# Kernel tuning notes

Hardware: AMD Instinct MI355X
Metric: run time of the kernel (lower is better)

## Reference

```python
import jax, jax.numpy as jnp
import numpy as np

B, H, W, DIM = 2, 128, 128, 256
HEADS, DHEAD = 16, 64
INNER = HEADS * DHEAD  # 1024
EPS = 1e-5  # BatchNorm eps


def _dwconv(x, w, groups):
    # x: [b, c_in, h, w], w: [c_out, c_in//groups, 3, 3], pad=1, stride=1
    return jax.lax.conv_general_dilated(
        x, w, window_strides=(1, 1), padding=((1, 1), (1, 1)),
        dimension_numbers=('NCHW', 'OIHW', 'NCHW'), feature_group_count=groups)


def _bn(x, gamma, beta, mean, var):
    # inference-mode BatchNorm2d over channel dim of NCHW
    inv = gamma * jax.lax.rsqrt(var + EPS)
    return (x - mean[None, :, None, None]) * inv[None, :, None, None] + beta[None, :, None, None]


def setup_inputs() -> dict:
    key = jax.random.key(0)
    ks = jax.random.split(key, 12)
    d = {}
    d['x_in'] = jax.random.normal(ks[0], (B, H, W, DIM), jnp.float32)
    def convw(k, cout):
        return jax.random.normal(k, (cout, 1, 3, 3), jnp.float32) * 0.1
    d['wq'] = convw(ks[1], INNER)
    d['wk'] = convw(ks[2], INNER)
    d['wv'] = convw(ks[3], INNER)
    for name, k in zip(('q', 'k', 'v'), (ks[4], ks[5], ks[6])):
        k0, k1 = jax.random.split(k)
        d[f'bn{name}_g'] = 1.0 + 0.1 * jax.random.normal(k0, (INNER,), jnp.float32)
        d[f'bn{name}_b'] = 0.05 * jax.random.normal(k1, (INNER,), jnp.float32)
        d[f'bn{name}_m'] = jnp.zeros((INNER,), jnp.float32)
        d[f'bn{name}_v'] = jnp.ones((INNER,), jnp.float32)
    d['rescale'] = jnp.ones((HEADS, 1, 1), jnp.float32)
    d['proj_w'] = jax.random.normal(ks[7], (DIM, INNER), jnp.float32) / np.sqrt(INNER).astype(np.float32)
    d['proj_b'] = jnp.zeros((DIM,), jnp.float32)
    d['pos_w1'] = convw(ks[8], DIM)
    d['pos_w2'] = convw(ks[9], DIM)
    return d


def _forward(x_in, wq, wk, wv,
             bnq_g, bnq_b, bnq_m, bnq_v,
             bnk_g, bnk_b, bnk_m, bnk_v,
             bnv_g, bnv_b, bnv_m, bnv_v,
             rescale, proj_w, proj_b, pos_w1, pos_w2):
    b, h, w, c = x_in.shape
    n = h * w
    x = jnp.transpose(x_in, (0, 3, 1, 2))  # [b, c, h, w]

    def proj_path(wc, g, be, m, va):
        y = _bn(_dwconv(x, wc, c), g, be, m, va)        # [b, INNER, h, w]
        return y.reshape(b, INNER, n).transpose(0, 2, 1)  # 'b c h w -> b (h w) c'

    q_inp = proj_path(wq, bnq_g, bnq_b, bnq_m, bnq_v)  # [b, n, INNER]
    k_inp = proj_path(wk, bnk_g, bnk_b, bnk_m, bnk_v)
    v_inp = proj_path(wv, bnv_g, bnv_b, bnv_m, bnv_v)

    def to_heads(t):
        # 'b n (h d) -> b h n d' then transpose(-2,-1) -> [b, heads, d, n]
        return t.reshape(b, n, HEADS, DHEAD).transpose(0, 2, 3, 1)

    q = to_heads(q_inp)
    k = to_heads(k_inp)
    v = to_heads(v_inp)
    # L2 normalize along token dim (last axis), torch F.normalize eps=1e-12
    q = q / jnp.clip(jnp.linalg.norm(q, axis=-1, keepdims=True), 1e-12)
    k = k / jnp.clip(jnp.linalg.norm(k, axis=-1, keepdims=True), 1e-12)

    attn = jnp.einsum('bhdn,bhen->bhde', k, q) * rescale[None]  # [b, heads, d, d]
    attn = jax.nn.softmax(attn, axis=-1)
    xo = jnp.einsum('bhde,bhen->bhdn', attn, v)  # [b, heads, d, n]
    # faithful to torch: raw reshape of [b, heads, d, n] -> [b, n, heads*d]
    xo = xo.reshape(b, n, HEADS * DHEAD)

    out_c = (xo @ proj_w.T + proj_b).reshape(b, h, w, c)

    vp = (v_inp @ proj_w.T + proj_b).reshape(b, h, w, c).transpose(0, 3, 1, 2)
    pe = _dwconv(jax.nn.gelu(_dwconv(vp, pos_w1, c), approximate=False), pos_w2, c)
    out_p = pe.transpose(0, 2, 3, 1)
    return out_c + out_p


def reference(x_in, wq, wk, wv,
              bnq_g, bnq_b, bnq_m, bnq_v,
              bnk_g, bnk_b, bnk_m, bnk_v,
              bnv_g, bnv_b, bnv_m, bnv_v,
              rescale, proj_w, proj_b, pos_w1, pos_w2):
    return _forward(x_in, wq, wk, wv,
                    bnq_g, bnq_b, bnq_m, bnq_v,
                    bnk_g, bnk_b, bnk_m, bnk_v,
                    bnv_g, bnv_b, bnv_m, bnv_v,
                    rescale, proj_w, proj_b, pos_w1, pos_w2)
```

## Files before the change

### kernel.cpp

```cpp
#include <hip/hip_runtime.h>

#define NTOK 16384
#define CDIM 256
#define INNER 1024
#define WW 128
#define HH 128

typedef unsigned short bf16_t;
typedef __bf16 bf16x8 __attribute__((ext_vector_type(8)));
typedef float f32x4 __attribute__((ext_vector_type(4)));

__device__ __forceinline__ float bf2f(bf16_t u) {
    union { unsigned int i; float f; } x;
    x.i = ((unsigned int)u) << 16;
    return x.f;
}
__device__ __forceinline__ bf16_t f2bf(float f) {
    union { float f; unsigned int i; } x;
    x.f = f;
    unsigned int r = x.i + 0x7FFFu + ((x.i >> 16) & 1u);
    return (bf16_t)(r >> 16);
}
__device__ __forceinline__ unsigned int cvtpk(float a, float b) {
    unsigned int r;
    asm("v_cvt_pk_bf16_f32 %0, %1, %2" : "=v"(r) : "v"(a), "v"(b));
    return r;
}

static const size_t OFF_XN   = 0;
static const size_t OFF_OUTC = 0;
static const size_t OFF_VT   = 16777216;
static const size_t OFF_XO   = 83886080;
static const size_t OFF_VP   = 150994944;
static const size_t OFF_PE2  = 184549376;
static const size_t OFF_WBF  = 201326592;
static const size_t OFF_S    = 218103808;
static const size_t OFF_SSQ  = 218628096;
static const size_t OFF_SSK  = 218636288;

__global__ __launch_bounds__(256) void k0_transpose(const float* __restrict__ x,
                                                    bf16_t* __restrict__ xn) {
    __shared__ bf16_t tile[32][33];
    int b = blockIdx.z;
    const float* xb = x + (size_t)b * NTOK * CDIM;
    bf16_t* xnb = xn + (size_t)b * CDIM * NTOK;
    int t0 = blockIdx.x * 32;
    int c0 = blockIdx.y * 32;
    int tx = threadIdx.x & 31, ty = threadIdx.x >> 5;
#pragma unroll
    for (int l = 0; l < 4; l++) {
        int t = t0 + ty + l * 8;
        tile[ty + l * 8][tx] = f2bf(xb[(size_t)t * CDIM + c0 + tx]);
    }
    __syncthreads();
#pragma unroll
    for (int l = 0; l < 4; l++) {
        int c = c0 + ty + l * 8;
        xnb[(size_t)c * NTOK + t0 + tx] = tile[tx][ty + l * 8];
    }
}

__global__ __launch_bounds__(512, 4) void k12_fused(
    const bf16_t* __restrict__ xn,
    const float* __restrict__ wq, const float* __restrict__ wk, const float* __restrict__ wv,
    const float* __restrict__ qg, const float* __restrict__ qb, const float* __restrict__ qm, const float* __restrict__ qv,
    const float* __restrict__ kg, const float* __restrict__ kb, const float* __restrict__ km, const float* __restrict__ kv_,
    const float* __restrict__ vg, const float* __restrict__ vb, const float* __restrict__ vm, const float* __restrict__ vv,
    bf16_t* __restrict__ vt, float* __restrict__ S,
    float* __restrict__ ssq, float* __restrict__ ssk) {
    int chunk = blockIdx.x;
    int h = blockIdx.y;
    int b = blockIdx.z;
    int y0 = chunk * 8;

    __shared__ ushort taps[16][10][132];
    __shared__ ushort Qs[64][72];
    __shared__ ushort Ks[64][72];
    __shared__ unsigned int Vs32[64][34];

    int tid = threadIdx.x;
    int lane = tid & 63, wave = tid >> 6;

    {
        const bf16_t* xb = xn + ((size_t)b * CDIM + (size_t)h * 16) * NTOK;
        for (int idx = tid; idx < 16 * 10 * 132; idx += 512) {
            int pp = idx / 1320;
            int rem = idx - pp * 1320;
            int i = rem / 132;
            int c = rem - i * 132;
            int gy = y0 - 1 + i, gx = c - 1;
            ushort val = 0;
            if (gy >= 0 && gy < HH && gx >= 0 && gx < WW)
                val = xb[(size_t)pp * NTOK + gy * WW + gx];
            taps[pp][i][c] = val;
        }
    }

    int tq = tid & 15;
    int pc = (tid >> 4) & 15;
    int ts = tid >> 8;

    const float* wsrc = ts ? wk : wq;
    const float* gp = ts ? kg : qg;
    const float* bp = ts ? kb : qb;
    const float* mp = ts ? km : qm;
    const float* vp_ = ts ? kv_ : qv;
    int chbase = h * 64 + pc * 4;
    float wQK[4][9], shQK[4];
#pragma unroll
    for (int s = 0; s < 4; s++) {
        int ch = chbase + s;
        float sc = gp[ch] * rsqrtf(vp_[ch] + 1e-5f);
        shQK[s] = bp[ch] - mp[ch] * sc;
#pragma unroll
        for (int t = 0; t < 9; t++) wQK[s][t] = wsrc[(size_t)ch * 9 + t] * sc;
    }
    float wV[2][9], shV[2];
#pragma unroll
    for (int sv = 0; sv < 2; sv++) {
        int ch = chbase + 2 * ts + sv;
        float sc = vg[ch] * rsqrtf(vv[ch] + 1e-5f);
        shV[sv] = vb[ch] - vm[ch] * sc;
#pragma unroll
        for (int t = 0; t < 9; t++) wV[sv][t] = wv[(size_t)ch * 9 + t] * sc;
    }

    ushort (*QK)[72] = ts ? Ks : Qs;

    int wm = wave & 1;
    int wn4 = wave >> 1;
    int qd = lane >> 4, l16 = lane & 15;
    f32x4 acc[2];
    acc[0] = (f32x4){0.f, 0.f, 0.f, 0.f};
    acc[1] = (f32x4){0.f, 0.f, 0.f, 0.f};

    int vrow = tid >> 3;
    int vseg = tid & 7;
    bf16_t* vtb = vt + (size_t)b * 16777216 + (size_t)h * 64;

    float ssl[4] = {0.f, 0.f, 0.f, 0.f};

    __syncthreads();

#pragma unroll 1
    for (int kc = 0; kc < 1024; kc += 64) {
        int grp = kc >> 6;
        int ly = grp >> 1;
        int xh = (grp & 1) << 6;
        int x0 = xh + tq * 4;

        float tp[3][6];
#pragma unroll
        for (int i = 0; i < 3; i++) {
            const ushort* rp = &taps[pc][ly + i][x0];
            ushort4 u4 = *(const ushort4*)rp;
            ushort2 u2 = *(const ushort2*)(rp + 4);
            tp[i][0] = bf2f(u4.x); tp[i][1] = bf2f(u4.y);
            tp[i][2] = bf2f(u4.z); tp[i][3] = bf2f(u4.w);
            tp[i][4] = bf2f(u2.x); tp[i][5] = bf2f(u2.y);
        }

#pragma unroll
        for (int s = 0; s < 4; s++) {
            float o0 = shQK[s], o1 = shQK[s], o2 = shQK[s], o3 = shQK[s];
#pragma unroll
            for (int i = 0; i < 3; i++) {
                float wa = wQK[s][i * 3 + 0], wb = wQK[s][i * 3 + 1], wc = wQK[s][i * 3 + 2];
                o0 += wa * tp[i][0] + wb * tp[i][1] + wc * tp[i][2];
                o1 += wa * tp[i][1] + wb * tp[i][2] + wc * tp[i][3];
                o2 += wa * tp[i][2] + wb * tp[i][3] + wc * tp[i][4];
                o3 += wa * tp[i][3] + wb * tp[i][4] + wc * tp[i][5];
            }
            ssl[s] += o0 * o0 + o1 * o1 + o2 * o2 + o3 * o3;
            uint2 pk;
            pk.x = cvtpk(o0, o1);
            pk.y = cvtpk(o2, o3);
            *(uint2*)&QK[pc * 4 + s][tq * 4] = pk;
        }

        {
            float ov[2][4];
#pragma unroll
            for (int sv = 0; sv < 2; sv++) {
                float o0 = shV[sv], o1 = shV[sv], o2 = shV[sv], o3 = shV[sv];
#pragma unroll
                for (int i = 0; i < 3; i++) {
                    float wa = wV[sv][i * 3 + 0], wb = wV[sv][i * 3 + 1], wc = wV[sv][i * 3 + 2];
                    o0 += wa * tp[i][0] + wb * tp[i][1] + wc * tp[i][2];
                    o1 += wa * tp[i][1] + wb * tp[i][2] + wc * tp[i][3];
                    o2 += wa * tp[i][2] + wb * tp[i][3] + wc * tp[i][4];
                    o3 += wa * tp[i][3] + wb * tp[i][4] + wc * tp[i][5];
                }
                ov[sv][0] = o0; ov[sv][1] = o1; ov[sv][2] = o2; ov[sv][3] = o3;
            }
#pragma unroll
            for (int j = 0; j < 4; j++)
                Vs32[tq * 4 + j][pc * 2 + ts] = cvtpk(ov[0][j], ov[1][j]);
        }

        __syncthreads();

        {
            uint4 o4;
            o4.x = Vs32[vrow][vseg * 4 + 0];
            o4.y = Vs32[vrow][vseg * 4 + 1];
            o4.z = Vs32[vrow][vseg * 4 + 2];
            o4.w = Vs32[vrow][vseg * 4 + 3];
            *(uint4*)&vtb[(size_t)(chunk * 1024 + kc + vrow) * 1024 + vseg * 8] = o4;
        }

#pragma unroll
        for (int kk = 0; kk < 64; kk += 32) {
            bf16x8 af0 = *(const bf16x8*)&Ks[wm * 32 + l16][kk + qd * 8];
            bf16x8 af1 = *(const bf16x8*)&Ks[wm * 32 + 16 + l16][kk + qd * 8];
            bf16x8 bf0 = *(const bf16x8*)&Qs[wn4 * 16 + l16][kk + qd * 8];
            acc[0] = __builtin_amdgcn_mfma_f32_16x16x32_bf16(af0, bf0, acc[0], 0, 0, 0);
            acc[1] = __builtin_amdgcn_mfma_f32_16x16x32_bf16(af1, bf0, acc[1], 0, 0, 0);
        }

        __syncthreads();
    }

    float* Sb = S + (size_t)(b * 16 + h) * 4096;
#pragma unroll
    for (int i = 0; i < 2; i++)
#pragma unroll
        for (int r = 0; r < 4; r++) {
            int d = wm * 32 + i * 16 + qd * 4 + r;
            int e = wn4 * 16 + l16;
            atomicAdd(&Sb[(size_t)d * 64 + e], acc[i][r]);
        }

#pragma unroll
    for (int s = 0; s < 4; s++) {
        float v = ssl[s];
#pragma unroll
        for (int o = 1; o < 16; o <<= 1) v += __shfl_xor(v, o, 64);
        ssl[s] = v;
    }
    if ((lane & 15) == 0) {
        float* dst = (ts ? ssk : ssq) + b * INNER + chbase;
        atomicAdd(&dst[0], ssl[0]);
        atomicAdd(&dst[1], ssl[1]);
        atomicAdd(&dst[2], ssl[2]);
        atomicAdd(&dst[3], ssl[3]);
    }
}

__global__ __launch_bounds__(64) void k3_softmax(float* __restrict__ S,
                                                 const float* __restrict__ ssq,
                                                 const float* __restrict__ ssk,
                                                 const float* __restrict__ rescale) {
    int bh = blockIdx.x;
    int b = bh >> 4, h = bh & 15;
    int d = threadIdx.x;
    __shared__ float rq[64];
    int cbase = b * INNER + h * 64;
    rq[d] = 1.0f / fmaxf(sqrtf(ssq[cbase + d]), 1e-12f);
    float rk = 1.0f / fmaxf(sqrtf(ssk[cbase + d]), 1e-12f);
    __syncthreads();
    float rsc = rescale[h];
    const float* row = S + (size_t)bh * 4096 + (size_t)d * 64;
    float sv[64];
    float mx = -3.4e38f;
#pragma unroll
    for (int e = 0; e < 64; e++) {
        sv[e] = row[e] * rk * rq[e] * rsc;
        mx = fmaxf(mx, sv[e]);
    }
    float sum = 0.f;
#pragma unroll
    for (int e = 0; e < 64; e++) {
        sv[e] = expf(sv[e] - mx);
        sum += sv[e];
    }
    float inv = 1.0f / sum;
    __syncthreads();
    ushort* attn = (ushort*)((char*)S + (size_t)bh * 16384);
#pragma unroll
    for (int e = 0; e < 64; e++) attn[d * 64 + e] = f2bf(sv[e] * inv);
}

__global__ __launch_bounds__(256) void cvt_w(const float* __restrict__ w,
                                             bf16_t* __restrict__ wbf) {
    int i = (blockIdx.x * 256 + threadIdx.x) * 4;
    float4 f = *(const float4*)&w[i];
    ushort4 r;
    r.x = f2bf(f.x); r.y = f2bf(f.y); r.z = f2bf(f.z); r.w = f2bf(f.w);
    *(ushort4*)&wbf[i] = r;
}

__global__ __launch_bounds__(256) void k4_mfma(const float* __restrict__ Sbase,
                                               const bf16_t* __restrict__ vt,
                                               bf16_t* __restrict__ xo) {
    int tt = blockIdx.x;
    int h = blockIdx.y;
    int b = blockIdx.z;
    int bh = b * 16 + h;
    const ushort* attn = (const ushort*)((const char*)Sbase + (size_t)bh * 16384);
    __shared__ ushort As[64][72];
    __shared__ ushort Bs[128][72];
    int tid = threadIdx.x, lane = tid & 63, wave = tid >> 6;
    int wm = wave & 1, wn = wave >> 1;
    int qd = lane >> 4, l16 = lane & 15;
    int r0 = tid >> 3, c0 = (tid & 7) * 8;
#pragma unroll
    for (int l = 0; l < 2; l++) {
        int row = r0 + l * 32;
        *(uint4*)&As[row][c0] = *(const uint4*)&attn[row * 64 + c0];
    }
    const bf16_t* vtb = vt + (size_t)b * 16777216 + (size_t)(tt * 128) * 1024 + h * 64;
#pragma unroll
    for (int l = 0; l < 4; l++) {
        int row = r0 + l * 32;
        *(uint4*)&Bs[row][c0] = *(const uint4*)&vtb[(size_t)row * 1024 + c0];
    }
    __syncthreads();
    f32x4 acc[2][4];
#pragma unroll
    for (int i = 0; i < 2; i++)
#pragma unroll
        for (int j = 0; j < 4; j++) acc[i][j] = (f32x4){0.f, 0.f, 0.f, 0.f};
#pragma unroll
    for (int kk = 0; kk < 64; kk += 32) {
        bf16x8 af[2], bfr[4];
#pragma unroll
        for (int i = 0; i < 2; i++)
            af[i] = *(const bf16x8*)&As[wm * 32 + i * 16 + l16][kk + qd * 8];
#pragma unroll
        for (int j = 0; j < 4; j++)
            bfr[j] = *(const bf16x8*)&Bs[wn * 64 + j * 16 + l16][kk + qd * 8];
#pragma unroll
        for (int i = 0; i < 2; i++)
#pragma unroll
            for (int j = 0; j < 4; j++)
                acc[i][j] = __builtin_amdgcn_mfma_f32_16x16x32_bf16(af[i], bfr[j], acc[i][j], 0, 0, 0);
    }
    bf16_t* xob = xo + (size_t)b * 16777216 + (size_t)(h * 64) * NTOK + (size_t)tt * 128;
#pragma unroll
    for (int i = 0; i < 2; i++)
#pragma unroll
        for (int j = 0; j < 4; j++)
#pragma unroll
            for (int r = 0; r < 4; r++) {
                int d = wm * 32 + i * 16 + qd * 4 + r;
                int t = wn * 64 + j * 16 + l16;
                xob[(size_t)d * NTOK + t] = f2bf(acc[i][j][r]);
            }
}

__global__ __launch_bounds__(256) void gemm_tn(
    const bf16_t* __restrict__ A, const bf16_t* __restrict__ B,
    const float* __restrict__ pb, bf16_t* __restrict__ C,
    int lda, int ldb, int ldc, int K,
    long strideA, long strideB, long strideC, int bias_on_n) {
    int mb = blockIdx.x, nb = blockIdx.y, b = blockIdx.z;
    A += (size_t)b * strideA;
    B += (size_t)b * strideB;
    C += (size_t)b * strideC;
    __shared__ ushort As[128][72];
    __shared__ ushort Bs[128][72];
    int tid = threadIdx.x;
    int lane = tid & 63, wave = tid >> 6;
    int wm = wave & 1, wn = wave >> 1;
    int q = lane >> 4, l16 = lane & 15;
    f32x4 acc[4][4];
#pragma unroll
    for (int i = 0; i < 4; i++)
#pragma unroll
        for (int j = 0; j < 4; j++) acc[i][j] = (f32x4){0.f, 0.f, 0.f, 0.f};
    const bf16_t* Ab = A + (size_t)mb * 128 * lda;
    const bf16_t* Bb = B + (size_t)nb * 128 * ldb;
    int r0 = tid >> 3;
    int c0 = (tid & 7) * 8;
#pragma unroll 1
    for (int kc = 0; kc < K; kc += 64) {
#pragma unroll
        for (int l = 0; l < 4; l++) {
            int row = l * 32 + r0;
            *(uint4*)&As[row][c0] = *(const uint4*)&Ab[(size_t)row * lda + kc + c0];
            *(uint4*)&Bs[row][c0] = *(const uint4*)&Bb[(size_t)row * ldb + kc + c0];
        }
        __syncthreads();
#pragma unroll
        for (int kk = 0; kk < 64; kk += 32) {
            bf16x8 af[4], bfr[4];
#pragma unroll
            for (int i = 0; i < 4; i++)
                af[i] = *(const bf16x8*)&As[wm * 64 + i * 16 + l16][kk + q * 8];
#pragma unroll
            for (int j = 0; j < 4; j++)
                bfr[j] = *(const bf16x8*)&Bs[wn * 64 + j * 16 + l16][kk + q * 8];
#pragma unroll
            for (int i = 0; i < 4; i++)
#pragma unroll
                for (int j = 0; j < 4; j++)
                    acc[i][j] = __builtin_amdgcn_mfma_f32_16x16x32_bf16(af[i], bfr[j], acc[i][j], 0, 0, 0);
        }
        __syncthreads();
    }
#pragma unroll
    for (int i = 0; i < 4; i++) {
#pragma unroll
        for (int j = 0; j < 4; j++) {
            int n = wn * 64 + j * 16 + l16;
            int gn = nb * 128 + n;
#pragma unroll
            for (int r = 0; r < 4; r++) {
                int m = wm * 64 + i * 16 + q * 4 + r;
                int gm = mb * 128 + m;
                float bias = bias_on_n ? pb[gn] : pb[gm];
                C[(size_t)gm * ldc + gn] = f2bf(acc[i][j][r] + bias);
            }
        }
    }
}

__global__ __launch_bounds__(256) void k_pos_fused(const bf16_t* __restrict__ vp,
                                                   const float* __restrict__ w1t,
                                                   const float* __restrict__ w2t,
                                                   bf16_t* __restrict__ pe2) {
    int ychunk = blockIdx.x;
    int ch = blockIdx.y;
    int b = blockIdx.z;
    int y0 = ychunk * 8;
    __shared__ float t1[12][132];
    __shared__ float t2[10][132];
    const bf16_t* plane = vp + (size_t)b * 4194304 + (size_t)ch * NTOK;
    for (int idx = threadIdx.x; idx < 12 * 132; idx += 256) {
        int i = idx / 132, c = idx % 132;
        int gy = y0 - 2 + i, gx = c - 2;
        float val = 0.f;
        if (gy >= 0 && gy < HH && gx >= 0 && gx < WW) val = bf2f(plane[gy * WW + gx]);
        t1[i][c] = val;
    }
    float wa[9], wb[9];
#pragma unroll
    for (int t = 0; t < 9; t++) {
        wa[t] = w1t[(size_t)ch * 9 + t];
        wb[t] = w2t[(size_t)ch * 9 + t];
    }
    __syncthreads();
    for (int idx = threadIdx.x; idx < 10 * 130; idx += 256) {
        int i = idx / 130, c1 = idx % 130;
        int yy = y0 - 1 + i, xx = c1 - 1;
        float val = 0.f;
        if (yy >= 0 && yy < HH && xx >= 0 && xx < WW) {
            float a = wa[0] * t1[i][c1]     + wa[1] * t1[i][c1 + 1]     + wa[2] * t1[i][c1 + 2]
                    + wa[3] * t1[i + 1][c1] + wa[4] * t1[i + 1][c1 + 1] + wa[5] * t1[i + 1][c1 + 2]
                    + wa[6] * t1[i + 2][c1] + wa[7] * t1[i + 2][c1 + 1] + wa[8] * t1[i + 2][c1 + 2];
            val = 0.5f * a * (1.0f + erff(a * 0.70710678118654752f));
        }
        t2[i][c1] = val;
    }
    __syncthreads();
    int x = threadIdx.x & 127;
    int half = threadIdx.x >> 7;
    bf16_t* oplane = pe2 + (size_t)b * 4194304 + (size_t)ch * NTOK;
#pragma unroll
    for (int rp = 0; rp < 4; rp++) {
        int r = rp * 2 + half;
        float acc = wb[0] * t2[r][x]     + wb[1] * t2[r][x + 1]     + wb[2] * t2[r][x + 2]
                  + wb[3] * t2[r + 1][x] + wb[4] * t2[r + 1][x + 1] + wb[5] * t2[r + 1][x + 2]
                  + wb[6] * t2[r + 2][x] + wb[7] * t2[r + 2][x + 1] + wb[8] * t2[r + 2][x + 2];
        oplane[(size_t)(y0 + r) * WW + x] = f2bf(acc);
    }
}

__global__ __launch_bounds__(256) void k9_final(const bf16_t* __restrict__ outc,
                                                const bf16_t* __restrict__ pe2,
                                                float* __restrict__ out) {
    __shared__ float tile[32][33];
    int t0 = blockIdx.x * 32;
    int c0 = blockIdx.y * 32;
    int b = blockIdx.z;
    int tx = threadIdx.x & 31, ty = threadIdx.x >> 5;
    const bf16_t* peb = pe2 + (size_t)b * 4194304;
    const bf16_t* ob = outc + (size_t)b * 4194304;
    float* o = out + (size_t)b * 4194304;
#pragma unroll
    for (int l = 0; l < 4; l++) {
        int c = c0 + ty + l * 8;
        tile[ty + l * 8][tx] = bf2f(peb[(size_t)c * NTOK + t0 + tx]);
    }
    __syncthreads();
#pragma unroll
    for (int l = 0; l < 4; l++) {
        int t = t0 + ty + l * 8;
        size_t idx = (size_t)t * CDIM + c0 + tx;
        o[idx] = bf2f(ob[idx]) + tile[tx][ty + l * 8];
    }
}

extern "C" void kernel_launch(void* const* d_in, const int* in_sizes, int n_in,
                              void* d_out, int out_size, void* d_ws, size_t ws_size,
                              hipStream_t stream) {
    const float* x_in    = (const float*)d_in[0];
    const float* wq      = (const float*)d_in[1];
    const float* wk      = (const float*)d_in[2];
    const float* wv      = (const float*)d_in[3];
    const float* qg      = (const float*)d_in[4];
    const float* qb      = (const float*)d_in[5];
    const float* qm      = (const float*)d_in[6];
    const float* qv      = (const float*)d_in[7];
    const float* kg      = (const float*)d_in[8];
    const float* kb      = (const float*)d_in[9];
    const float* km      = (const float*)d_in[10];
    const float* kv_     = (const float*)d_in[11];
    const float* vg      = (const float*)d_in[12];
    const float* vb      = (const float*)d_in[13];
    const float* vm      = (const float*)d_in[14];
    const float* vv      = (const float*)d_in[15];
    const float* rescale = (const float*)d_in[16];
    const float* proj_w  = (const float*)d_in[17];
    const float* proj_b  = (const float*)d_in[18];
    const float* pos_w1  = (const float*)d_in[19];
    const float* pos_w2  = (const float*)d_in[20];

    char* ws = (char*)d_ws;
    bf16_t* xn   = (bf16_t*)(ws + OFF_XN);
    bf16_t* vt   = (bf16_t*)(ws + OFF_VT);
    bf16_t* xo   = (bf16_t*)(ws + OFF_XO);
    bf16_t* outc = (bf16_t*)(ws + OFF_OUTC);
    bf16_t* vp   = (bf16_t*)(ws + OFF_VP);
    bf16_t* pe2  = (bf16_t*)(ws + OFF_PE2);
    bf16_t* wbf  = (bf16_t*)(ws + OFF_WBF);
    float* S     = (float*)(ws + OFF_S);
    float* ssq   = (float*)(ws + OFF_SSQ);
    float* ssk   = (float*)(ws + OFF_SSK);

    hipMemsetAsync(ws + OFF_S, 0, (size_t)540672, stream);

    k0_transpose<<<dim3(512, 8, 2), 256, 0, stream>>>(x_in, xn);
    k12_fused<<<dim3(16, 16, 2), 512, 0, stream>>>(xn, wq, wk, wv,
                                                   qg, qb, qm, qv,
                                                   kg, kb, km, kv_,
                                                   vg, vb, vm, vv,
                                                   vt, S, ssq, ssk);
    k3_softmax<<<dim3(32), 64, 0, stream>>>(S, ssq, ssk, rescale);
    cvt_w<<<dim3(256), 256, 0, stream>>>(proj_w, wbf);
    k4_mfma<<<dim3(128, 16, 2), 256, 0, stream>>>(S, vt, xo);
    gemm_tn<<<dim3(128, 2, 2), 256, 0, stream>>>(xo, wbf, proj_b, outc,
                                                 1024, 1024, 256, 1024,
                                                 16777216L, 0L, 4194304L, 1);
    gemm_tn<<<dim3(2, 128, 2), 256, 0, stream>>>(wbf, vt, proj_b, vp,
                                                 1024, 1024, 16384, 1024,
                                                 0L, 16777216L, 4194304L, 0);
    k_pos_fused<<<dim3(16, 256, 2), 256, 0, stream>>>(vp, pos_w1, pos_w2, pe2);
    k9_final<<<dim3(512, 8, 2), 256, 0, stream>>>(outc, pe2, (float*)d_out);
}
```

Before: 342.2 us.

## Fuse input transpose into conv kernel and final add into output GEMM epilogue

Removes the standalone transpose kernel: the fused conv/QK kernel now reads the NHWC fp32 input directly with float4 loads and converts to bf16 while filling its shared tap tiles. Removes the final add kernel by reordering launches so the output projection GEMM runs after the positional branch and adds the transposed pe2 tile (staged through shared memory) plus bias in its epilogue, writing fp32 output directly. This cuts two launches and the intermediate outc/xn round trips, at the cost of strided, less coalesced input loads in the conv kernel and scattered fp32 stores in the GEMM epilogue.

```diff
diff --git a/kernel.cpp b/kernel.cpp
--- a/kernel.cpp
+++ b/kernel.cpp
@@ -27,8 +27,6 @@
     return r;
 }
 
-static const size_t OFF_XN   = 0;
-static const size_t OFF_OUTC = 0;
 static const size_t OFF_VT   = 16777216;
 static const size_t OFF_XO   = 83886080;
 static const size_t OFF_VP   = 150994944;
@@ -38,30 +36,8 @@
 static const size_t OFF_SSQ  = 218628096;
 static const size_t OFF_SSK  = 218636288;
 
-__global__ __launch_bounds__(256) void k0_transpose(const float* __restrict__ x,
-                                                    bf16_t* __restrict__ xn) {
-    __shared__ bf16_t tile[32][33];
-    int b = blockIdx.z;
-    const float* xb = x + (size_t)b * NTOK * CDIM;
-    bf16_t* xnb = xn + (size_t)b * CDIM * NTOK;
-    int t0 = blockIdx.x * 32;
-    int c0 = blockIdx.y * 32;
-    int tx = threadIdx.x & 31, ty = threadIdx.x >> 5;
-#pragma unroll
-    for (int l = 0; l < 4; l++) {
-        int t = t0 + ty + l * 8;
-        tile[ty + l * 8][tx] = f2bf(xb[(size_t)t * CDIM + c0 + tx]);
-    }
-    __syncthreads();
-#pragma unroll
-    for (int l = 0; l < 4; l++) {
-        int c = c0 + ty + l * 8;
-        xnb[(size_t)c * NTOK + t0 + tx] = tile[tx][ty + l * 8];
-    }
-}
-
 __global__ __launch_bounds__(512, 4) void k12_fused(
-    const bf16_t* __restrict__ xn,
+    const float* __restrict__ x,
     const float* __restrict__ wq, const float* __restrict__ wk, const float* __restrict__ wv,
     const float* __restrict__ qg, const float* __restrict__ qb, const float* __restrict__ qm, const float* __restrict__ qv,
     const float* __restrict__ kg, const float* __restrict__ kb, const float* __restrict__ km, const float* __restrict__ kv_,
@@ -82,17 +58,23 @@
     int lane = tid & 63, wave = tid >> 6;
 
     {
-        const bf16_t* xb = xn + ((size_t)b * CDIM + (size_t)h * 16) * NTOK;
-        for (int idx = tid; idx < 16 * 10 * 132; idx += 512) {
-            int pp = idx / 1320;
-            int rem = idx - pp * 1320;
-            int i = rem / 132;
-            int c = rem - i * 132;
+        const float* xb = x + (size_t)b * NTOK * CDIM + h * 16;
+        for (int u = tid; u < 5200; u += 512) {
+            int pos = u >> 2, quad = u & 3;
+            int i = pos / 130, c = pos - i * 130;
             int gy = y0 - 1 + i, gx = c - 1;
-            ushort val = 0;
-            if (gy >= 0 && gy < HH && gx >= 0 && gx < WW)
-                val = xb[(size_t)pp * NTOK + gy * WW + gx];
-            taps[pp][i][c] = val;
+            if (gy >= 0 && gy < HH && gx >= 0 && gx < WW) {
+                float4 v = *(const float4*)&xb[(size_t)(gy * WW + gx) * CDIM + quad * 4];
+                taps[quad * 4 + 0][i][c] = f2bf(v.x);
+                taps[quad * 4 + 1][i][c] = f2bf(v.y);
+                taps[quad * 4 + 2][i][c] = f2bf(v.z);
+                taps[quad * 4 + 3][i][c] = f2bf(v.w);
+            } else {
+                taps[quad * 4 + 0][i][c] = 0;
+                taps[quad * 4 + 1][i][c] = 0;
+                taps[quad * 4 + 2][i][c] = 0;
+                taps[quad * 4 + 3][i][c] = 0;
+            }
         }
     }
 
@@ -349,17 +331,19 @@
             }
 }
 
+template <int FUSE_PE2>
 __global__ __launch_bounds__(256) void gemm_tn(
     const bf16_t* __restrict__ A, const bf16_t* __restrict__ B,
-    const float* __restrict__ pb, bf16_t* __restrict__ C,
+    const float* __restrict__ pb, void* __restrict__ Cv,
     int lda, int ldb, int ldc, int K,
-    long strideA, long strideB, long strideC, int bias_on_n) {
+    long strideA, long strideB, long strideC, int bias_on_n,
+    const bf16_t* __restrict__ pe2) {
     int mb = blockIdx.x, nb = blockIdx.y, b = blockIdx.z;
     A += (size_t)b * strideA;
     B += (size_t)b * strideB;
-    C += (size_t)b * strideC;
-    __shared__ ushort As[128][72];
-    __shared__ ushort Bs[128][72];
+    __shared__ ushort smem[2 * 128 * 72];
+    ushort (*As)[72] = (ushort(*)[72])smem;
+    ushort (*Bs)[72] = (ushort(*)[72])(smem + 128 * 72);
     int tid = threadIdx.x;
     int lane = tid & 63, wave = tid >> 6;
     int wm = wave & 1, wn = wave >> 1;
@@ -399,18 +383,47 @@
         }
         __syncthreads();
     }
-#pragma unroll
-    for (int i = 0; i < 4; i++) {
-#pragma unroll
-        for (int j = 0; j < 4; j++) {
-            int n = wn * 64 + j * 16 + l16;
-            int gn = nb * 128 + n;
-#pragma unroll
-            for (int r = 0; r < 4; r++) {
-                int m = wm * 64 + i * 16 + q * 4 + r;
-                int gm = mb * 128 + m;
-                float bias = bias_on_n ? pb[gn] : pb[gm];
-                C[(size_t)gm * ldc + gn] = f2bf(acc[i][j][r] + bias);
+    if (FUSE_PE2) {
+        const bf16_t* peb = pe2 + (size_t)b * 4194304;
+        int gm0 = mb * 128, gn0 = nb * 128;
+        for (int u = tid; u < 128 * 16; u += 256) {
+            int row = u >> 4, seg = u & 15;
+            *(uint4*)&smem[row * 132 + seg * 8] =
+                *(const uint4*)&peb[(size_t)(gn0 + row) * NTOK + gm0 + seg * 8];
+        }
+        __syncthreads();
+        float* C = (float*)Cv + (size_t)b * strideC;
+#pragma unroll
+        for (int i = 0; i < 4; i++) {
+#pragma unroll
+            for (int j = 0; j < 4; j++) {
+                int n = wn * 64 + j * 16 + l16;
+                int gn = gn0 + n;
+                int m0 = wm * 64 + i * 16 + q * 4;
+                ushort4 pv4 = *(const ushort4*)&smem[n * 132 + m0];
+                float bias = pb[gn];
+#pragma unroll
+                for (int r = 0; r < 4; r++) {
+                    ushort pu = (r == 0) ? pv4.x : ((r == 1) ? pv4.y : ((r == 2) ? pv4.z : pv4.w));
+                    C[(size_t)(gm0 + m0 + r) * ldc + gn] = acc[i][j][r] + bias + bf2f(pu);
+                }
+            }
+        }
+    } else {
+        bf16_t* C = (bf16_t*)Cv + (size_t)b * strideC;
+#pragma unroll
+        for (int i = 0; i < 4; i++) {
+#pragma unroll
+            for (int j = 0; j < 4; j++) {
+                int n = wn * 64 + j * 16 + l16;
+                int gn = nb * 128 + n;
+#pragma unroll
+                for (int r = 0; r < 4; r++) {
+                    int m = wm * 64 + i * 16 + q * 4 + r;
+                    int gm = mb * 128 + m;
+                    float bias = bias_on_n ? pb[gn] : pb[gm];
+                    C[(size_t)gm * ldc + gn] = f2bf(acc[i][j][r] + bias);
+                }
             }
         }
     }
@@ -464,31 +477,6 @@
                   + wb[3] * t2[r + 1][x] + wb[4] * t2[r + 1][x + 1] + wb[5] * t2[r + 1][x + 2]
                   + wb[6] * t2[r + 2][x] + wb[7] * t2[r + 2][x + 1] + wb[8] * t2[r + 2][x + 2];
         oplane[(size_t)(y0 + r) * WW + x] = f2bf(acc);
-    }
-}
-
-__global__ __launch_bounds__(256) void k9_final(const bf16_t* __restrict__ outc,
-                                                const bf16_t* __restrict__ pe2,
-                                                float* __restrict__ out) {
-    __shared__ float tile[32][33];
-    int t0 = blockIdx.x * 32;
-    int c0 = blockIdx.y * 32;
-    int b = blockIdx.z;
-    int tx = threadIdx.x & 31, ty = threadIdx.x >> 5;
-    const bf16_t* peb = pe2 + (size_t)b * 4194304;
-    const bf16_t* ob = outc + (size_t)b * 4194304;
-    float* o = out + (size_t)b * 4194304;
-#pragma unroll
-    for (int l = 0; l < 4; l++) {
-        int c = c0 + ty + l * 8;
-        tile[ty + l * 8][tx] = bf2f(peb[(size_t)c * NTOK + t0 + tx]);
-    }
-    __syncthreads();
-#pragma unroll
-    for (int l = 0; l < 4; l++) {
-        int t = t0 + ty + l * 8;
-        size_t idx = (size_t)t * CDIM + c0 + tx;
-        o[idx] = bf2f(ob[idx]) + tile[tx][ty + l * 8];
     }
 }
 
@@ -518,10 +506,8 @@
     const float* pos_w2  = (const float*)d_in[20];
 
     char* ws = (char*)d_ws;
-    bf16_t* xn   = (bf16_t*)(ws + OFF_XN);
     bf16_t* vt   = (bf16_t*)(ws + OFF_VT);
     bf16_t* xo   = (bf16_t*)(ws + OFF_XO);
-    bf16_t* outc = (bf16_t*)(ws + OFF_OUTC);
     bf16_t* vp   = (bf16_t*)(ws + OFF_VP);
     bf16_t* pe2  = (bf16_t*)(ws + OFF_PE2);
     bf16_t* wbf  = (bf16_t*)(ws + OFF_WBF);
@@ -531,8 +517,7 @@
 
     hipMemsetAsync(ws + OFF_S, 0, (size_t)540672, stream);
 
-    k0_transpose<<<dim3(512, 8, 2), 256, 0, stream>>>(x_in, xn);
-    k12_fused<<<dim3(16, 16, 2), 512, 0, stream>>>(xn, wq, wk, wv,
+    k12_fused<<<dim3(16, 16, 2), 512, 0, stream>>>(x_in, wq, wk, wv,
                                                    qg, qb, qm, qv,
                                                    kg, kb, km, kv_,
                                                    vg, vb, vm, vv,
@@ -540,12 +525,11 @@
     k3_softmax<<<dim3(32), 64, 0, stream>>>(S, ssq, ssk, rescale);
     cvt_w<<<dim3(256), 256, 0, stream>>>(proj_w, wbf);
     k4_mfma<<<dim3(128, 16, 2), 256, 0, stream>>>(S, vt, xo);
-    gemm_tn<<<dim3(128, 2, 2), 256, 0, stream>>>(xo, wbf, proj_b, outc,
-                                                 1024, 1024, 256, 1024,
-                                                 16777216L, 0L, 4194304L, 1);
-    gemm_tn<<<dim3(2, 128, 2), 256, 0, stream>>>(wbf, vt, proj_b, vp,
-                                                 1024, 1024, 16384, 1024,
-                                                 0L, 16777216L, 4194304L, 0);
+    gemm_tn<0><<<dim3(2, 128, 2), 256, 0, stream>>>(wbf, vt, proj_b, vp,
+                                                    1024, 1024, 16384, 1024,
+                                                    0L, 16777216L, 4194304L, 0, nullptr);
     k_pos_fused<<<dim3(16, 256, 2), 256, 0, stream>>>(vp, pos_w1, pos_w2, pe2);
-    k9_final<<<dim3(512, 8, 2), 256, 0, stream>>>(outc, pe2, (float*)d_out);
-}
+    gemm_tn<1><<<dim3(128, 2, 2), 256, 0, stream>>>(xo, wbf, proj_b, d_out,
+                                                    1024, 1024, 256, 1024,
+                                                    16777216L, 0L, 4194304L, 1, pe2);
+}
```

Measured after the change: 318.2 us. 1.08x faster.
